# Performance work log

Hardware: AMD Instinct MI355X
Metric: run time of the kernel (lower is better)

Reference implementation:

```python
import jax, jax.numpy as jnp
import numpy as np

B, F, V, D, H = 16384, 45, 10000, 256, 32


def setup_inputs() -> dict:
    key = jax.random.key(0)
    ks = jax.random.split(key, 6)
    src = jax.random.randint(ks[0], (B, F), 0, V, dtype=jnp.int64 if jax.config.jax_enable_x64 else jnp.int32)
    tables = jax.random.normal(ks[1], (F, V, D), dtype=jnp.float32) * 0.02
    W1 = jax.random.normal(ks[2], (D, H), dtype=jnp.float32) * 0.05
    b1 = jax.random.normal(ks[3], (H,), dtype=jnp.float32) * 0.05
    W2 = jax.random.normal(ks[4], (H, 1), dtype=jnp.float32) * 0.05
    b2 = jax.random.normal(ks[5], (1,), dtype=jnp.float32) * 0.05
    return {"src": src, "tables": tables, "W1": W1, "b1": b1, "W2": W2, "b2": b2}


def reference(src, tables, W1, b1, W2, b2):
    # Fused multi-table gather: emb[b, f] = tables[f, src[b, f]]  -> [B, F, D]
    feat_idx = jnp.arange(F)[None, :]            # [1, F]
    emb = tables[feat_idx, src]                  # [B, F, D]
    # Small MLP applied per feature position, then sum over features.
    h = jnp.einsum('bfd,dh->bfh', emb, W1) + b1  # [B, F, 32]
    out = jnp.einsum('bfh,ho->bfo', h, W2) + b2  # [B, F, 1]
    return jnp.sum(out, axis=1)                  # [B, 1]
```

## Files before the change

### kernel.cpp

```cpp
#include <hip/hip_runtime.h>


#define BN 16384
#define FN 45
#define VN 10000
#define DN 256
#define HN 32
#define RN (FN * VN)

__global__ void prep_kernel(const float* __restrict__ W1,
                            const float* __restrict__ b1,
                            const float* __restrict__ W2,
                            const float* __restrict__ b2,
                            float* __restrict__ w_out,
                            float* __restrict__ c_out) {
    const int d = threadIdx.x;
    float s = 0.f;
#pragma unroll
    for (int h = 0; h < HN; ++h) s += W1[d * HN + h] * W2[h];
    w_out[d] = s;
    if (d == 0) {
        float cc = 0.f;
#pragma unroll
        for (int h = 0; h < HN; ++h) cc += b1[h] * W2[h];
        c_out[0] = (float)FN * (cc + b2[0]);
    }
}

__global__ void scatter_kernel(const int* __restrict__ src,
                               unsigned char* __restrict__ flags) {
    const int i = blockIdx.x * blockDim.x + threadIdx.x;
    const int f = i % FN;
    flags[f * VN + src[i]] = (unsigned char)1;
}

__global__ void row_dot_kernel(const float* __restrict__ tables,
                               const float* __restrict__ w_glob,
                               const unsigned char* __restrict__ flags,
                               float* __restrict__ t) {
    __shared__ __align__(16) float w_s[DN];
    w_s[threadIdx.x] = w_glob[threadIdx.x];
    __syncthreads();

    const int r = blockIdx.x * blockDim.x + threadIdx.x;
    if (r >= RN) return;
    if (!flags[r]) return;

    const float4* __restrict__ row =
        reinterpret_cast<const float4*>(tables + (size_t)r * DN);
    const float4* __restrict__ wv4 = reinterpret_cast<const float4*>(w_s);
    float s = 0.f;
#pragma unroll
    for (int j = 0; j < DN / 4; ++j) {
        const float4 v = row[j];
        const float4 wv = wv4[j];
        s += v.x * wv.x + v.y * wv.y + v.z * wv.z + v.w * wv.w;
    }
    t[r] = s;
}

__global__ void gather_kernel(const int* __restrict__ src,
                              const float* __restrict__ t,
                              const float* __restrict__ c,
                              float* __restrict__ out) {
    const int b = blockIdx.x * blockDim.x + threadIdx.x;
    const int* __restrict__ s_row = src + (size_t)b * FN;
    float s = 0.f;
#pragma unroll
    for (int f = 0; f < FN; ++f) {
        s += t[f * VN + s_row[f]];
    }
    out[b] = s + c[0];
}

extern "C" void kernel_launch(void* const* d_in, const int* in_sizes, int n_in,
                              void* d_out, int out_size, void* d_ws, size_t ws_size,
                              hipStream_t stream) {
    const int* src = (const int*)d_in[0];
    const float* tables = (const float*)d_in[1];
    const float* W1 = (const float*)d_in[2];
    const float* b1 = (const float*)d_in[3];
    const float* W2 = (const float*)d_in[4];
    const float* b2 = (const float*)d_in[5];
    float* out = (float*)d_out;

    float* t = (float*)d_ws;
    float* w = t + RN;
    float* c = w + DN;
    unsigned char* flags = (unsigned char*)(c + 1);

    prep_kernel<<<1, 256, 0, stream>>>(W1, b1, W2, b2, w, c);
    hipMemsetAsync(flags, 0, RN, stream);
    scatter_kernel<<<(BN * FN) / 256, 256, 0, stream>>>(src, flags);
    row_dot_kernel<<<(RN + 255) / 256, 256, 0, stream>>>(tables, w, flags, t);
    gather_kernel<<<BN / 256, 256, 0, stream>>>(src, t, c, out);
}
```

Before: 630.8 us.

## Coalesce row dot products with wavefront-per-8-rows and 64-bit flag checks

```diff
diff --git a/kernel.cpp b/kernel.cpp
--- a/kernel.cpp
+++ b/kernel.cpp
@@ -34,29 +34,44 @@
     flags[f * VN + src[i]] = (unsigned char)1;
 }
 
-__global__ void row_dot_kernel(const float* __restrict__ tables,
-                               const float* __restrict__ w_glob,
-                               const unsigned char* __restrict__ flags,
-                               float* __restrict__ t) {
-    __shared__ __align__(16) float w_s[DN];
-    w_s[threadIdx.x] = w_glob[threadIdx.x];
-    __syncthreads();
+__global__ __launch_bounds__(256)
+void row_dot_kernel(const float* __restrict__ tables,
+                    const float* __restrict__ w_glob,
+                    const unsigned long long* __restrict__ flags8,
+                    float* __restrict__ t) {
+    const int lane = threadIdx.x & 63;
+    const int g = (blockIdx.x * blockDim.x + threadIdx.x) >> 6;
+    const int r0 = g * 8;
+    if (r0 >= RN) return;
 
-    const int r = blockIdx.x * blockDim.x + threadIdx.x;
-    if (r >= RN) return;
-    if (!flags[r]) return;
+    const float4 wv = reinterpret_cast<const float4*>(w_glob)[lane];
 
-    const float4* __restrict__ row =
-        reinterpret_cast<const float4*>(tables + (size_t)r * DN);
-    const float4* __restrict__ wv4 = reinterpret_cast<const float4*>(w_s);
-    float s = 0.f;
+    const unsigned long long fl = flags8[g];
+    if (fl == 0ull) return;
+
+    const float4* __restrict__ base =
+        reinterpret_cast<const float4*>(tables) + (size_t)r0 * (DN / 4);
+
+    float4 v[8];
 #pragma unroll
-    for (int j = 0; j < DN / 4; ++j) {
-        const float4 v = row[j];
-        const float4 wv = wv4[j];
-        s += v.x * wv.x + v.y * wv.y + v.z * wv.z + v.w * wv.w;
+    for (int k = 0; k < 8; ++k) {
+        if ((fl >> (8 * k)) & 0xFFull) v[k] = base[k * (DN / 4) + lane];
     }
-    t[r] = s;
+    float s[8];
+#pragma unroll
+    for (int k = 0; k < 8; ++k) {
+        if ((fl >> (8 * k)) & 0xFFull) {
+            s[k] = v[k].x * wv.x + v[k].y * wv.y + v[k].z * wv.z + v[k].w * wv.w;
+        }
+    }
+#pragma unroll
+    for (int k = 0; k < 8; ++k) {
+        if ((fl >> (8 * k)) & 0xFFull) {
+#pragma unroll
+            for (int m = 1; m < 64; m <<= 1) s[k] += __shfl_xor(s[k], m);
+            if (lane == 0) t[r0 + k] = s[k];
+        }
+    }
 }
 
 __global__ void gather_kernel(const int* __restrict__ src,
@@ -85,13 +100,14 @@
     float* out = (float*)d_out;
 
     float* t = (float*)d_ws;
-    float* w = t + RN;
+    unsigned char* flags = (unsigned char*)d_ws + (size_t)RN * 4;
+    float* w = (float*)((unsigned char*)d_ws + (size_t)RN * 5);
     float* c = w + DN;
-    unsigned char* flags = (unsigned char*)(c + 1);
 
     prep_kernel<<<1, 256, 0, stream>>>(W1, b1, W2, b2, w, c);
     hipMemsetAsync(flags, 0, RN, stream);
     scatter_kernel<<<(BN * FN) / 256, 256, 0, stream>>>(src, flags);
-    row_dot_kernel<<<(RN + 255) / 256, 256, 0, stream>>>(tables, w, flags, t);
+    row_dot_kernel<<<(RN / 8 + 3) / 4, 256, 0, stream>>>(
+        tables, w, (const unsigned long long*)flags, t);
     gather_kernel<<<BN / 256, 256, 0, stream>>>(src, t, c, out);
 }
```

Result: faster. 606.5 us (-3.8%).
